# Kernel tuning notes

Hardware: AMD Instinct MI355X
Metric: run time of the kernel (lower is better)

Reference implementation:

```python
import jax, jax.numpy as jnp
import numpy as np

N_NODES = 50000
N_EDGES = 800000
HID = 128

def _silu(x):
    return x * jax.nn.sigmoid(x)

def setup_inputs() -> dict:
    key = jax.random.key(0)
    ks = jax.random.split(key, 8)
    s = lambda fan_in: 1.0 / np.sqrt(fan_in)
    return {
        "h": jax.random.normal(ks[0], (N_NODES, HID), jnp.float32),
        "edges": jax.random.randint(ks[1], (2, N_EDGES), 0, N_NODES, jnp.int64),
        "distances": jax.random.uniform(ks[2], (N_EDGES, 1), jnp.float32),
        "W_e1": jax.random.normal(ks[3], (2 * HID + 1, HID), jnp.float32) * s(2 * HID + 1),
        "b_e1": jnp.zeros((HID,), jnp.float32),
        "W_e2": jax.random.normal(ks[4], (HID, HID), jnp.float32) * s(HID),
        "b_e2": jnp.zeros((HID,), jnp.float32),
        "W_ei": jax.random.normal(ks[5], (HID, 1), jnp.float32) * s(HID),
        "b_ei": jnp.zeros((1,), jnp.float32),
        "W_n1": jax.random.normal(ks[6], (HID + 1, HID), jnp.float32) * s(HID + 1),
        "b_n1": jnp.zeros((HID,), jnp.float32),
        "W_n2": jax.random.normal(ks[7], (HID, HID), jnp.float32) * s(HID),
        "b_n2": jnp.zeros((HID,), jnp.float32),
    }

def reference(h, edges, distances, W_e1, b_e1, W_e2, b_e2, W_ei, b_ei, W_n1, b_n1, W_n2, b_n2):
    row, col = edges[0], edges[1]
    # edge MLP + sigmoid gate (computed as in original; output unused downstream)
    einp = jnp.concatenate([h[row], h[col], distances], axis=1)   # [E, 2H+1]
    m = _silu(einp @ W_e1 + b_e1)
    m = _silu(m @ W_e2 + b_e2)
    edge_feat = jax.nn.sigmoid(m @ W_ei + b_ei) * m               # [E, H]
    del edge_feat  # original forward never consumes it
    # scatter-add of distances into per-node aggregate, scaled by 1/100
    agg = jax.ops.segment_sum(distances, row, num_segments=h.shape[0]) / 100.0  # [N, 1]
    # node update MLP with residual
    ninp = jnp.concatenate([h, agg], axis=-1)                      # [N, H+1]
    u = _silu(ninp @ W_n1 + b_n1) @ W_n2 + b_n2
    return h + u
```

## Files before the change

kernel.cpp:

```cpp
#include <hip/hip_runtime.h>

#define HID 128
#define NODE_PAD 50048
#define NRANGE 4
#define RANGE 12512
#define NPART 64
#define NGRP 8

typedef __attribute__((ext_vector_type(8))) short short8;
typedef __attribute__((ext_vector_type(4))) float floatx4;

__device__ __forceinline__ short f2bf(float f) {
    unsigned u = __builtin_bit_cast(unsigned, f);
    unsigned r = (u + 0x7FFFu + ((u >> 16) & 1u)) >> 16;
    return (short)r;
}
__device__ __forceinline__ float bf2f(short s) {
    unsigned u = ((unsigned)(unsigned short)s) << 16;
    return __builtin_bit_cast(float, u);
}

__global__ __launch_bounds__(1024) void scatter_lds(const int* __restrict__ rows,
                                                    const float* __restrict__ dist,
                                                    unsigned short* __restrict__ part,
                                                    int n_edges) {
    __shared__ float bins[RANGE];
    const int i = blockIdx.x;
    const int b = (i & 7) * (NPART / 8) + (i >> 5);
    const int r = (i >> 3) & (NRANGE - 1);
    const int base = r * RANGE;

    for (int t = threadIdx.x; t < RANGE / 4; t += 1024)
        ((float4*)bins)[t] = make_float4(0.f, 0.f, 0.f, 0.f);
    __syncthreads();

    const int chunk = (n_edges + NPART - 1) / NPART;
    const int cbeg = b * chunk;
    const int cend = min(cbeg + chunk, n_edges);

    for (int e = cbeg + threadIdx.x * 4; e < cend; e += 1024 * 4) {
        if (e + 4 <= cend) {
            int4   rr = *(const int4*)(rows + e);
            float4 dd = *(const float4*)(dist + e);
            if ((unsigned)(rr.x - base) < RANGE) atomicAdd(&bins[rr.x - base], dd.x);
            if ((unsigned)(rr.y - base) < RANGE) atomicAdd(&bins[rr.y - base], dd.y);
            if ((unsigned)(rr.z - base) < RANGE) atomicAdd(&bins[rr.z - base], dd.z);
            if ((unsigned)(rr.w - base) < RANGE) atomicAdd(&bins[rr.w - base], dd.w);
        } else {
            for (int j = e; j < cend; ++j) {
                int rw = rows[j];
                if ((unsigned)(rw - base) < RANGE) atomicAdd(&bins[rw - base], dist[j]);
            }
        }
    }
    __syncthreads();

    unsigned short* dst = part + (size_t)b * NODE_PAD + base;
    for (int t = threadIdx.x; t < RANGE / 8; t += 1024) {
        float4 lo = ((const float4*)bins)[t * 2];
        float4 hi = ((const float4*)bins)[t * 2 + 1];
        short8 v;
        v[0] = f2bf(lo.x); v[1] = f2bf(lo.y); v[2] = f2bf(lo.z); v[3] = f2bf(lo.w);
        v[4] = f2bf(hi.x); v[5] = f2bf(hi.y); v[6] = f2bf(hi.z); v[7] = f2bf(hi.w);
        *(short8*)(dst + t * 8) = v;
    }
}

__global__ __launch_bounds__(256) void reduce_partials(
    const unsigned short* __restrict__ part,
    float* __restrict__ agg4) {
    const int g   = blockIdx.x & (NGRP - 1);
    const int idx = (blockIdx.x >> 3) * 256 + threadIdx.x;
    const int n8  = NODE_PAD / 8;
    if (idx < n8) {
        float s[8] = {0.f, 0.f, 0.f, 0.f, 0.f, 0.f, 0.f, 0.f};
#pragma unroll
        for (int c = 0; c < NPART / NGRP; ++c) {
            const unsigned short* p =
                part + (size_t)(g * (NPART / NGRP) + c) * NODE_PAD + idx * 8;
            short8 v = *(const short8*)p;
#pragma unroll
            for (int j = 0; j < 8; ++j) s[j] += bf2f(v[j]);
        }
        float* o = agg4 + (size_t)g * NODE_PAD + idx * 8;
        *(float4*)o       = make_float4(s[0], s[1], s[2], s[3]);
        *(float4*)(o + 4) = make_float4(s[4], s[5], s[6], s[7]);
    }
}

__global__ __launch_bounds__(512) void node_mlp_mfma(
    const float* __restrict__ h,
    const float* __restrict__ agg4,
    const float* __restrict__ W1,
    const float* __restrict__ b1,
    const float* __restrict__ W2,
    const float* __restrict__ b2,
    float* __restrict__ out,
    int n_nodes)
{
    __shared__ short WL[128 * 136];
    __shared__ short t_lds[8][16 * 136];

    const int tid  = threadIdx.x;
    const int wv   = tid >> 6;
    const int lane = tid & 63;
    const int m16  = lane & 15;
    const int quad = lane >> 4;
    const int node0 = blockIdx.x * 128 + wv * 16;

    short8 a1[4];
    {
        int row = node0 + m16;
        if (row >= n_nodes) row = n_nodes - 1;
        const float* hr = h + (size_t)row * HID + quad * 8;
#pragma unroll
        for (int kc = 0; kc < 4; ++kc) {
            float4 x0 = *(const float4*)(hr + kc * 32);
            float4 x1 = *(const float4*)(hr + kc * 32 + 4);
            short8 v;
            v[0] = f2bf(x0.x); v[1] = f2bf(x0.y); v[2] = f2bf(x0.z); v[3] = f2bf(x0.w);
            v[4] = f2bf(x1.x); v[5] = f2bf(x1.y); v[6] = f2bf(x1.z); v[7] = f2bf(x1.w);
            a1[kc] = v;
        }
    }

    float4 a4;
    {
        float4 s = make_float4(0.f, 0.f, 0.f, 0.f);
#pragma unroll
        for (int g = 0; g < NGRP; ++g) {
            float4 p = *(const float4*)(agg4 + (size_t)g * NODE_PAD + node0 + quad * 4);
            s.x += p.x; s.y += p.y; s.z += p.z; s.w += p.w;
        }
        a4.x = s.x * 0.01f; a4.y = s.y * 0.01f; a4.z = s.z * 0.01f; a4.w = s.w * 0.01f;
    }

    const int kg = tid >> 5;
    const int cc = tid & 31;

    {
        const float* src = W1 + (size_t)(kg * 8) * HID + cc * 4;
        float r[8][4];
#pragma unroll
        for (int j = 0; j < 8; ++j)
            *(float4*)r[j] = *(const float4*)(src + j * HID);
#pragma unroll
        for (int jj = 0; jj < 4; ++jj) {
            short8 v;
#pragma unroll
            for (int j = 0; j < 8; ++j) v[j] = f2bf(r[j][jj]);
            *(short8*)(WL + (cc * 4 + jj) * 136 + kg * 8) = v;
        }
    }
    __syncthreads();

#pragma unroll
    for (int nt = 0; nt < 8; ++nt) {
        floatx4 acc = {0.f, 0.f, 0.f, 0.f};
        const short* wb = WL + (nt * 16 + m16) * 136 + quad * 8;
#pragma unroll
        for (int kc = 0; kc < 4; ++kc) {
            short8 bfr = *(const short8*)(wb + kc * 32);
            acc = __builtin_amdgcn_mfma_f32_16x16x32_bf16(a1[kc], bfr, acc, 0, 0, 0);
        }
        int col = nt * 16 + m16;
        float bias = b1[col];
        float wagg = W1[(size_t)HID * HID + col];
        float av[4] = {a4.x, a4.y, a4.z, a4.w};
#pragma unroll
        for (int r = 0; r < 4; ++r) {
            float v = acc[r] + bias + av[r] * wagg;
            float sg = __builtin_amdgcn_rcpf(1.0f + __expf(-v));
            v *= sg;
            t_lds[wv][(quad * 4 + r) * 136 + col] = f2bf(v);
        }
    }

    __syncthreads();

    {
        const float* src = W2 + (size_t)(kg * 8) * HID + cc * 4;
        float r[8][4];
#pragma unroll
        for (int j = 0; j < 8; ++j)
            *(float4*)r[j] = *(const float4*)(src + j * HID);
#pragma unroll
        for (int jj = 0; jj < 4; ++jj) {
            short8 v;
#pragma unroll
            for (int j = 0; j < 8; ++j) v[j] = f2bf(r[j][jj]);
            *(short8*)(WL + (cc * 4 + jj) * 136 + kg * 8) = v;
        }
    }
    __syncthreads();

    short8 a2[4];
#pragma unroll
    for (int kc = 0; kc < 4; ++kc)
        a2[kc] = *(const short8*)(&t_lds[wv][m16 * 136 + kc * 32 + quad * 8]);

    float b2v[8];
#pragma unroll
    for (int nt = 0; nt < 8; ++nt) b2v[nt] = b2[nt * 16 + m16];

    float* scratch = (float*)&t_lds[wv][0];
    const int erow = lane & 15;
    const int ecg  = lane >> 4;
#pragma unroll
    for (int nt = 0; nt < 8; ++nt) {
        floatx4 acc = {0.f, 0.f, 0.f, 0.f};
        const short* wb = WL + (nt * 16 + m16) * 136 + quad * 8;
#pragma unroll
        for (int kc = 0; kc < 4; ++kc) {
            short8 bfr = *(const short8*)(wb + kc * 32);
            acc = __builtin_amdgcn_mfma_f32_16x16x32_bf16(a2[kc], bfr, acc, 0, 0, 0);
        }
#pragma unroll
        for (int r = 0; r < 4; ++r)
            scratch[(quad * 4 + r) * 17 + m16] = acc[r] + b2v[nt];
        float4 sv = *(const float4*)(scratch + erow * 17 + ecg * 4);
        int row = node0 + erow;
        if (row < n_nodes) {
            size_t off = (size_t)row * HID + nt * 16 + ecg * 4;
            float4 hv = *(const float4*)(h + off);
            float4 o = make_float4(hv.x + sv.x, hv.y + sv.y,
                                   hv.z + sv.z, hv.w + sv.w);
            *(float4*)(out + off) = o;
        }
    }
}

extern "C" void kernel_launch(void* const* d_in, const int* in_sizes, int n_in,
                              void* d_out, int out_size, void* d_ws, size_t ws_size,
                              hipStream_t stream) {
    const float* h     = (const float*)d_in[0];
    const int*   edges = (const int*)d_in[1];
    const float* dist  = (const float*)d_in[2];
    const float* W1    = (const float*)d_in[9];
    const float* b1    = (const float*)d_in[10];
    const float* W2    = (const float*)d_in[11];
    const float* b2    = (const float*)d_in[12];
    float* out = (float*)d_out;

    const int n_nodes = in_sizes[0] / HID;
    const int n_edges = in_sizes[2];
    const int* rows = edges;

    unsigned short* part = (unsigned short*)d_ws;
    float* agg4 = (float*)(part + (size_t)NPART * NODE_PAD);

    scatter_lds<<<NRANGE * NPART, 1024, 0, stream>>>(rows, dist, part, n_edges);

    reduce_partials<<<NGRP * ((NODE_PAD / 8 + 255) / 256), 256, 0, stream>>>(part, agg4);

    const int blocks = (n_nodes + 127) / 128;
    node_mlp_mfma<<<blocks, 512, 0, stream>>>(h, agg4, W1, b1, W2, b2, out, n_nodes);
}
```

Before: 122.6 us.

## Pre-transpose weights to bf16 once and read them from global in the node MLP

Two extra blocks in the reduce kernel convert W1 and W2 to transposed bf16 copies in workspace. The node MLP then reads MFMA B-fragments straight from those global copies instead of each of its ~391 blocks converting and staging both weight matrices into LDS with barriers. This drops 34 KB of LDS per block and three __syncthreads, which can raise occupancy. The cost is B loads from L2/global (128x128 bf16, likely cached) inside the MFMA loops instead of LDS reads.

```diff
diff --git a/kernel.cpp b/kernel.cpp
--- a/kernel.cpp
+++ b/kernel.cpp
@@ -6,6 +6,7 @@
 #define RANGE 12512
 #define NPART 64
 #define NGRP 8
+#define NRED (NGRP * ((NODE_PAD / 8 + 255) / 256))
 
 typedef __attribute__((ext_vector_type(8))) short short8;
 typedef __attribute__((ext_vector_type(4))) float floatx4;
@@ -68,7 +69,26 @@
 
 __global__ __launch_bounds__(256) void reduce_partials(
     const unsigned short* __restrict__ part,
-    float* __restrict__ agg4) {
+    float* __restrict__ agg4,
+    const float* __restrict__ W1,
+    const float* __restrict__ W2,
+    unsigned short* __restrict__ WT1,
+    unsigned short* __restrict__ WT2) {
+    if (blockIdx.x >= NRED) {
+        const float* W = (blockIdx.x == NRED) ? W1 : W2;
+        unsigned short* WT = (blockIdx.x == NRED) ? WT1 : WT2;
+        const int col = threadIdx.x & 127;
+        const int kh  = (threadIdx.x >> 7) * 64;
+#pragma unroll
+        for (int k8 = 0; k8 < 8; ++k8) {
+            short8 v;
+#pragma unroll
+            for (int j = 0; j < 8; ++j)
+                v[j] = f2bf(W[(size_t)(kh + k8 * 8 + j) * HID + col]);
+            *(short8*)(WT + (size_t)col * HID + kh + k8 * 8) = v;
+        }
+        return;
+    }
     const int g   = blockIdx.x & (NGRP - 1);
     const int idx = (blockIdx.x >> 3) * 256 + threadIdx.x;
     const int n8  = NODE_PAD / 8;
@@ -91,14 +111,14 @@
 __global__ __launch_bounds__(512) void node_mlp_mfma(
     const float* __restrict__ h,
     const float* __restrict__ agg4,
+    const unsigned short* __restrict__ WT1,
+    const unsigned short* __restrict__ WT2,
     const float* __restrict__ W1,
     const float* __restrict__ b1,
-    const float* __restrict__ W2,
     const float* __restrict__ b2,
     float* __restrict__ out,
     int n_nodes)
 {
-    __shared__ short WL[128 * 136];
     __shared__ short t_lds[8][16 * 136];
 
     const int tid  = threadIdx.x;
@@ -135,73 +155,39 @@
         a4.x = s.x * 0.01f; a4.y = s.y * 0.01f; a4.z = s.z * 0.01f; a4.w = s.w * 0.01f;
     }
 
-    const int kg = tid >> 5;
-    const int cc = tid & 31;
-
-    {
-        const float* src = W1 + (size_t)(kg * 8) * HID + cc * 4;
-        float r[8][4];
-#pragma unroll
-        for (int j = 0; j < 8; ++j)
-            *(float4*)r[j] = *(const float4*)(src + j * HID);
-#pragma unroll
-        for (int jj = 0; jj < 4; ++jj) {
-            short8 v;
-#pragma unroll
-            for (int j = 0; j < 8; ++j) v[j] = f2bf(r[j][jj]);
-            *(short8*)(WL + (cc * 4 + jj) * 136 + kg * 8) = v;
-        }
-    }
-    __syncthreads();
+    float b1v[8], waggv[8], b2v[8];
+#pragma unroll
+    for (int nt = 0; nt < 8; ++nt) {
+        int col = nt * 16 + m16;
+        b1v[nt]   = b1[col];
+        waggv[nt] = W1[(size_t)HID * HID + col];
+        b2v[nt]   = b2[col];
+    }
 
 #pragma unroll
     for (int nt = 0; nt < 8; ++nt) {
         floatx4 acc = {0.f, 0.f, 0.f, 0.f};
-        const short* wb = WL + (nt * 16 + m16) * 136 + quad * 8;
+        const unsigned short* wb = WT1 + (size_t)(nt * 16 + m16) * HID + quad * 8;
 #pragma unroll
         for (int kc = 0; kc < 4; ++kc) {
             short8 bfr = *(const short8*)(wb + kc * 32);
             acc = __builtin_amdgcn_mfma_f32_16x16x32_bf16(a1[kc], bfr, acc, 0, 0, 0);
         }
+        float av[4] = {a4.x, a4.y, a4.z, a4.w};
         int col = nt * 16 + m16;
-        float bias = b1[col];
-        float wagg = W1[(size_t)HID * HID + col];
-        float av[4] = {a4.x, a4.y, a4.z, a4.w};
 #pragma unroll
         for (int r = 0; r < 4; ++r) {
-            float v = acc[r] + bias + av[r] * wagg;
+            float v = acc[r] + b1v[nt] + av[r] * waggv[nt];
             float sg = __builtin_amdgcn_rcpf(1.0f + __expf(-v));
             v *= sg;
             t_lds[wv][(quad * 4 + r) * 136 + col] = f2bf(v);
         }
     }
 
-    __syncthreads();
-
-    {
-        const float* src = W2 + (size_t)(kg * 8) * HID + cc * 4;
-        float r[8][4];
-#pragma unroll
-        for (int j = 0; j < 8; ++j)
-            *(float4*)r[j] = *(const float4*)(src + j * HID);
-#pragma unroll
-        for (int jj = 0; jj < 4; ++jj) {
-            short8 v;
-#pragma unroll
-            for (int j = 0; j < 8; ++j) v[j] = f2bf(r[j][jj]);
-            *(short8*)(WL + (cc * 4 + jj) * 136 + kg * 8) = v;
-        }
-    }
-    __syncthreads();
-
     short8 a2[4];
 #pragma unroll
     for (int kc = 0; kc < 4; ++kc)
         a2[kc] = *(const short8*)(&t_lds[wv][m16 * 136 + kc * 32 + quad * 8]);
-
-    float b2v[8];
-#pragma unroll
-    for (int nt = 0; nt < 8; ++nt) b2v[nt] = b2[nt * 16 + m16];
 
     float* scratch = (float*)&t_lds[wv][0];
     const int erow = lane & 15;
@@ -209,7 +195,7 @@
 #pragma unroll
     for (int nt = 0; nt < 8; ++nt) {
         floatx4 acc = {0.f, 0.f, 0.f, 0.f};
-        const short* wb = WL + (nt * 16 + m16) * 136 + quad * 8;
+        const unsigned short* wb = WT2 + (size_t)(nt * 16 + m16) * HID + quad * 8;
 #pragma unroll
         for (int kc = 0; kc < 4; ++kc) {
             short8 bfr = *(const short8*)(wb + kc * 32);
@@ -248,11 +234,13 @@
 
     unsigned short* part = (unsigned short*)d_ws;
     float* agg4 = (float*)(part + (size_t)NPART * NODE_PAD);
+    unsigned short* WT1 = (unsigned short*)(agg4 + (size_t)NGRP * NODE_PAD);
+    unsigned short* WT2 = WT1 + HID * HID;
 
     scatter_lds<<<NRANGE * NPART, 1024, 0, stream>>>(rows, dist, part, n_edges);
 
-    reduce_partials<<<NGRP * ((NODE_PAD / 8 + 255) / 256), 256, 0, stream>>>(part, agg4);
+    reduce_partials<<<NRED + 2, 256, 0, stream>>>(part, agg4, W1, W2, WT1, WT2);
 
     const int blocks = (n_nodes + 127) / 128;
-    node_mlp_mfma<<<blocks, 512, 0, stream>>>(h, agg4, W1, b1, W2, b2, out, n_nodes);
-}
+    node_mlp_mfma<<<blocks, 512, 0, stream>>>(h, agg4, WT1, WT2, W1, b1, b2, out, n_nodes);
+}
```

New measurement: 147.0 us. 1.2x slower.
